# Kernel tuning notes

Hardware: AMD Instinct MI355X
Metric: run time of the kernel (lower is better)

The kernel has to match this reference:

```python
import jax, jax.numpy as jnp
import numpy as np

N = 50000        # nodes
E = 400000       # edges
SC = 64          # scalar (l=0) channels
VC = 32          # vector (l=1) channels
DIM = SC + 3 * VC  # 160
NB = 64          # radial basis functions
CUTOFF = 5.0
EPS = 1e-5


def _edge_rot_mat(edge_vec, edge_rand):
    # init_edge_rot_mat: build per-edge frame aligning edge dir with canonical axis
    dist = jnp.sqrt(jnp.sum(edge_vec ** 2, axis=1, keepdims=True))
    nx = edge_vec / dist
    ev2 = edge_rand - 0.5
    ev2 = ev2 / jnp.sqrt(jnp.sum(ev2 ** 2, axis=1, keepdims=True))
    ev2b = jnp.stack([-ev2[:, 1], ev2[:, 0], ev2[:, 2]], axis=1)
    ev2c = jnp.stack([ev2[:, 0], -ev2[:, 2], ev2[:, 1]], axis=1)
    dot = lambda a: jnp.abs(jnp.sum(a * nx, axis=1, keepdims=True))
    ev2 = jnp.where(dot(ev2) > dot(ev2b), ev2b, ev2)
    ev2 = jnp.where(dot(ev2) > dot(ev2c), ev2c, ev2)
    nz = jnp.cross(nx, ev2)
    nz = nz / jnp.sqrt(jnp.sum(nz ** 2, axis=1, keepdims=True))
    ny = jnp.cross(nx, nz)
    ny = ny / jnp.sqrt(jnp.sum(ny ** 2, axis=1, keepdims=True))
    # edge_rot_mat_inv columns = [nz, nx, -ny]; R = inv^T -> rows = [nz, nx, -ny]
    return jnp.stack([nz, nx, -ny], axis=1)  # [E,3,3]


def setup_inputs() -> dict:
    key = jax.random.key(0)
    ks = jax.random.split(key, 10)
    x = jax.random.normal(ks[0], (N, DIM), dtype=jnp.float32)
    pos = jax.random.normal(ks[1], (N, 3), dtype=jnp.float32)
    src = jax.random.randint(ks[2], (E,), 0, N)
    off = jax.random.randint(ks[3], (E,), 1, N)
    dst = (src + off) % N  # no self loops -> nonzero edge vectors
    edge_index = jnp.stack([src, dst], axis=0).astype(jnp.int64)
    edge_rand = jax.random.uniform(ks[4], (E, 3), dtype=jnp.float32)
    W0 = jax.random.normal(ks[5], (SC, SC), dtype=jnp.float32)
    W1 = jax.random.normal(ks[6], (VC, VC), dtype=jnp.float32)
    rbf_centers = jnp.linspace(0.0, CUTOFF, NB).astype(jnp.float32)
    rbf_widths = 0.5 * jnp.ones((NB,), dtype=jnp.float32)
    edge_proj_w = 0.1 * jax.random.normal(ks[7], (NB, 1), dtype=jnp.float32)
    edge_proj_b = jnp.zeros((1,), dtype=jnp.float32)
    ln_gamma = jnp.ones((SC,), dtype=jnp.float32) + 0.1 * jax.random.normal(ks[8], (SC,), dtype=jnp.float32)
    ln_beta = 0.1 * jax.random.normal(ks[9], (SC,), dtype=jnp.float32)
    return {"x": x, "pos": pos, "edge_index": edge_index, "edge_rand": edge_rand,
            "W0": W0, "W1": W1, "rbf_centers": rbf_centers, "rbf_widths": rbf_widths,
            "edge_proj_w": edge_proj_w, "edge_proj_b": edge_proj_b,
            "ln_gamma": ln_gamma, "ln_beta": ln_beta}


def reference(x, pos, edge_index, edge_rand, W0, W1, rbf_centers, rbf_widths,
              edge_proj_w, edge_proj_b, ln_gamma, ln_beta):
    src, dst = edge_index[0], edge_index[1]
    edge_vec = pos[src] - pos[dst]                       # [E,3]
    dist = jnp.sqrt(jnp.sum(edge_vec ** 2, axis=1))      # [E]
    # rotation matrices are detached in the original
    R = jax.lax.stop_gradient(_edge_rot_mat(edge_vec, edge_rand))  # [E,3,3]

    # radial basis (gaussian) with cosine cutoff envelope
    d = dist[:, None]                                    # [E,1]
    rbf = jnp.exp(-0.5 * ((d - rbf_centers) / rbf_widths) ** 2)  # [E,NB]
    cut = jnp.where(d <= CUTOFF, 0.5 * (jnp.cos(jnp.pi * d / CUTOFF) + 1.0), 0.0)
    rbf = rbf * cut                                      # [E,NB]

    # gather source features, split irreps 64x0e + 32x1e
    h = x[src]                                           # [E,DIM]
    h0 = h[:, :SC]                                       # [E,SC]
    h1 = h[:, SC:].reshape(-1, VC, 3)                    # [E,VC,3]

    # rotate l=1 block into the edge-aligned frame (Wigner-D for l=1 is R)
    h1r = jnp.einsum('eij,ecj->eci', R, h1)

    # SO2 convolution: per-l channel mixing (o3.Linear, 1/sqrt(fan_in) path norm)
    m0 = (h0 @ W0) / np.sqrt(SC)                         # [E,SC]
    m1 = jnp.einsum('ecj,cd->edj', h1r, W1) / np.sqrt(VC)  # [E,VC,3]

    # edge modulation: global mean of sigmoid(edge_proj(rbf)) (scalar, as in source)
    edge_w = jnp.mean(jax.nn.sigmoid(rbf @ edge_proj_w + edge_proj_b))
    m0 = m0 * edge_w
    m1 = m1 * edge_w

    # rotate l=1 back with R^T
    m1b = jnp.einsum('eji,ecj->eci', R, m1)
    msg = jnp.concatenate([m0, m1b.reshape(-1, 3 * VC)], axis=1)  # [E,DIM]

    # scatter-sum aggregation over destination nodes
    agg = jax.ops.segment_sum(msg, dst, num_segments=x.shape[0])  # [N,DIM]

    # EquivariantLayerNormV2: LayerNorm on l=0 slice only
    s = agg[:, :SC]
    mu = jnp.mean(s, axis=-1, keepdims=True)
    var = jnp.mean((s - mu) ** 2, axis=-1, keepdims=True)
    s_ln = (s - mu) / jnp.sqrt(var + EPS) * ln_gamma + ln_beta

    # S2Activation: SiLU on l=0 slice, identity on l=1
    s_act = jax.nn.silu(s_ln)
    return jnp.concatenate([s_act, agg[:, SC:]], axis=1)  # [N,DIM]
```

## Files before the change

kernel.cpp:

```cpp
#include <hip/hip_runtime.h>

#define N_NODES 50000
#define N_EDGES 400000
#define DIM 160
#define NB 64
#define CUTOFF 5.0f
#define LN_EPS 1e-5f
#define PI_F 3.14159265358979323846f

#define SLOT_STRIDE 64
#define DEG_STRIDE 8

#define WS_DEG   16
#define WS_PKT   (WS_DEG + N_NODES * DEG_STRIDE)
#define WS_POS4  (WS_PKT + 4 * NB)
#define WS_ESRC  (WS_POS4 + 4 * N_NODES)

__global__ __launch_bounds__(256) void prep(
    const float* __restrict__ pos, const float* __restrict__ centers,
    const float* __restrict__ widths, const float* __restrict__ proj_w,
    int* __restrict__ degp, float4* __restrict__ pkt,
    float4* __restrict__ pos4, float* __restrict__ ew_accum)
{
    const int i = blockIdx.x * blockDim.x + threadIdx.x;
    if (i < 16) ((int*)ew_accum)[i] = 0;
    if (i < NB)
        pkt[i] = make_float4(centers[i], 1.0f / widths[i], proj_w[i], 0.0f);
    if (i < N_NODES) {
        const int4 z4 = make_int4(0, 0, 0, 0);
        ((int4*)(degp))[2 * i]     = z4;
        ((int4*)(degp))[2 * i + 1] = z4;
        pos4[i] = make_float4(pos[3 * i], pos[3 * i + 1], pos[3 * i + 2], 0.0f);
    }
}

#define EPT 4

__global__ __launch_bounds__(256) void hist_ew_fill(
    const int* __restrict__ ei, const float4* __restrict__ pos4,
    const float4* __restrict__ pkt, const float* __restrict__ proj_b,
    int* __restrict__ degp, int* __restrict__ esrc, float* __restrict__ ew_accum)
{
    const float bias = proj_b[0];
    const int base = blockIdx.x * (256 * EPT) + threadIdx.x;

    int  s[EPT], d[EPT], slot[EPT];
    bool v[EPT];
    #pragma unroll
    for (int k = 0; k < EPT; ++k) {
        const int e = base + 256 * k;
        v[k] = (e < N_EDGES);
        s[k] = v[k] ? ei[e] : 0;
        d[k] = v[k] ? ei[N_EDGES + e] : 0;
    }

    #pragma unroll
    for (int k = 0; k < EPT; ++k)
        slot[k] = v[k] ? atomicAdd(&degp[(long)d[k] * DEG_STRIDE], 1) : 0;

    float4 ps[EPT], pd[EPT];
    #pragma unroll
    for (int k = 0; k < EPT; ++k) { ps[k] = pos4[s[k]]; pd[k] = pos4[d[k]]; }

    #pragma unroll
    for (int k = 0; k < EPT; ++k)
        if (v[k] && slot[k] < SLOT_STRIDE)
            esrc[((long)d[k] << 6) + slot[k]] = s[k];

    float dist[EPT];
    #pragma unroll
    for (int k = 0; k < EPT; ++k) {
        const float dx = ps[k].x - pd[k].x;
        const float dy = ps[k].y - pd[k].y;
        const float dz = ps[k].z - pd[k].z;
        dist[k] = sqrtf(dx * dx + dy * dy + dz * dz);
    }

    float z[EPT] = {0.f, 0.f, 0.f, 0.f};
    #pragma unroll 4
    for (int b = 0; b < NB; ++b) {
        const float4 t4 = pkt[b];
        #pragma unroll
        for (int k = 0; k < EPT; ++k) {
            const float t = (dist[k] - t4.x) * t4.y;
            z[k] = fmaf(__expf(-0.5f * t * t), t4.z, z[k]);
        }
    }

    float sig = 0.0f;
    #pragma unroll
    for (int k = 0; k < EPT; ++k) {
        if (v[k]) {
            const float cut = (dist[k] <= CUTOFF)
                            ? 0.5f * (__cosf(PI_F * dist[k] * (1.0f / CUTOFF)) + 1.0f)
                            : 0.0f;
            sig += 1.0f / (1.0f + __expf(-(z[k] * cut + bias)));
        }
    }

    #pragma unroll
    for (int off = 32; off > 0; off >>= 1) sig += __shfl_xor(sig, off);
    __shared__ float red[4];
    if ((threadIdx.x & 63) == 0) red[threadIdx.x >> 6] = sig;
    __syncthreads();
    if (threadIdx.x == 0)
        atomicAdd(ew_accum, red[0] + red[1] + red[2] + red[3]);
}

#define TNODES 16

__global__ __launch_bounds__(256) void gather_node(
    const float* __restrict__ x, const int* __restrict__ degp,
    const int* __restrict__ esrc, float* __restrict__ out,
    const float* __restrict__ W0, const float* __restrict__ W1,
    const float* __restrict__ ln_gamma, const float* __restrict__ ln_beta,
    const float* __restrict__ ew_accum)
{
    __shared__ float sW0[64 * 64];
    __shared__ float sW1[32 * 32];
    __shared__ float sRow[4][2][160];

    const int t    = threadIdx.x;
    const int lane = t & 63;
    const int w    = t >> 6;
    const int node0 = blockIdx.x * TNODES;

    {
        const float4* w04 = (const float4*)W0;
        float4* s04 = (float4*)sW0;
        #pragma unroll
        for (int i = 0; i < 4; ++i) s04[t + 256 * i] = w04[t + 256 * i];
        ((float4*)sW1)[t] = ((const float4*)W1)[t];
    }
    __syncthreads();

    const float ew   = ew_accum[0] * (1.0f / 400000.0f);
    const float s_m0 = ew * 0.125f;
    const float s_m1 = ew * 0.17677669529663687f;

    const int half = lane >> 5;
    const int l    = lane & 31;

    #pragma unroll 1
    for (int p = 0; p < 4; p += 2) {
        const int nA  = node0 + 4 * w + p;
        const int nB  = nA + 1;
        const long nAc = (nA < N_NODES) ? nA : 0;
        const long nBc = (nB < N_NODES) ? nB : 0;

        const int svA  = esrc[(nAc << 6) + lane];
        const int svB  = esrc[(nBc << 6) + lane];
        const int cntA = (nA < N_NODES) ? min(degp[nAc * DEG_STRIDE], SLOT_STRIDE) : 0;
        const int cntB = (nB < N_NODES) ? min(degp[nBc * DEG_STRIDE], SLOT_STRIDE) : 0;

        float4 aA = make_float4(0.f, 0.f, 0.f, 0.f);
        float4 aB = make_float4(0.f, 0.f, 0.f, 0.f);

        #define GBODY(sv, cnt, acc)                                            \
        {                                                                      \
            int j = 0;                                                         \
            for (; j + 8 <= cnt; j += 8) {                                     \
                const int s0 = __shfl(sv, j);                                  \
                const int s1 = __shfl(sv, j + 1);                              \
                const int s2 = __shfl(sv, j + 2);                              \
                const int s3 = __shfl(sv, j + 3);                              \
                const int s4 = __shfl(sv, j + 4);                              \
                const int s5 = __shfl(sv, j + 5);                              \
                const int s6 = __shfl(sv, j + 6);                              \
                const int s7 = __shfl(sv, j + 7);                              \
                if (lane < 40) {                                               \
                    const float4 v0 = ((const float4*)(x + (long)s0 * DIM))[lane]; \
                    const float4 v1 = ((const float4*)(x + (long)s1 * DIM))[lane]; \
                    const float4 v2 = ((const float4*)(x + (long)s2 * DIM))[lane]; \
                    const float4 v3 = ((const float4*)(x + (long)s3 * DIM))[lane]; \
                    const float4 v4 = ((const float4*)(x + (long)s4 * DIM))[lane]; \
                    const float4 v5 = ((const float4*)(x + (long)s5 * DIM))[lane]; \
                    const float4 v6 = ((const float4*)(x + (long)s6 * DIM))[lane]; \
                    const float4 v7 = ((const float4*)(x + (long)s7 * DIM))[lane]; \
                    acc.x += ((v0.x + v1.x) + (v2.x + v3.x)) + ((v4.x + v5.x) + (v6.x + v7.x)); \
                    acc.y += ((v0.y + v1.y) + (v2.y + v3.y)) + ((v4.y + v5.y) + (v6.y + v7.y)); \
                    acc.z += ((v0.z + v1.z) + (v2.z + v3.z)) + ((v4.z + v5.z) + (v6.z + v7.z)); \
                    acc.w += ((v0.w + v1.w) + (v2.w + v3.w)) + ((v4.w + v5.w) + (v6.w + v7.w)); \
                }                                                              \
            }                                                                  \
            for (; j + 4 <= cnt; j += 4) {                                     \
                const int s0 = __shfl(sv, j);                                  \
                const int s1 = __shfl(sv, j + 1);                              \
                const int s2 = __shfl(sv, j + 2);                              \
                const int s3 = __shfl(sv, j + 3);                              \
                if (lane < 40) {                                               \
                    const float4 v0 = ((const float4*)(x + (long)s0 * DIM))[lane]; \
                    const float4 v1 = ((const float4*)(x + (long)s1 * DIM))[lane]; \
                    const float4 v2 = ((const float4*)(x + (long)s2 * DIM))[lane]; \
                    const float4 v3 = ((const float4*)(x + (long)s3 * DIM))[lane]; \
                    acc.x += (v0.x + v1.x) + (v2.x + v3.x);                    \
                    acc.y += (v0.y + v1.y) + (v2.y + v3.y);                    \
                    acc.z += (v0.z + v1.z) + (v2.z + v3.z);                    \
                    acc.w += (v0.w + v1.w) + (v2.w + v3.w);                    \
                }                                                              \
            }                                                                  \
            for (; j < cnt; ++j) {                                             \
                const int s0 = __shfl(sv, j);                                  \
                if (lane < 40) {                                               \
                    const float4 v0 = ((const float4*)(x + (long)s0 * DIM))[lane]; \
                    acc.x += v0.x; acc.y += v0.y; acc.z += v0.z; acc.w += v0.w; \
                }                                                              \
            }                                                                  \
        }
        GBODY(svA, cntA, aA)
        GBODY(svB, cntB, aB)
        #undef GBODY

        if (lane < 40) {
            *(float4*)(&sRow[w][0][4 * lane]) = aA;
            *(float4*)(&sRow[w][1][4 * lane]) = aB;
        }

        const int  node  = node0 + 4 * w + p + half;
        const bool valid = node < N_NODES;
        float* grow = out + (long)(valid ? node : 0) * DIM;
        const float* row = &sRow[w][half][0];

        {
            float a0 = 0.f, a1 = 0.f;
            #pragma unroll 4
            for (int k0 = 0; k0 < 64; k0 += 4) {
                const float4 a = *(const float4*)(row + k0);
                const float2 q0 = *(const float2*)(sW0 + (k0 + 0) * 64 + 2 * l);
                const float2 q1 = *(const float2*)(sW0 + (k0 + 1) * 64 + 2 * l);
                const float2 q2 = *(const float2*)(sW0 + (k0 + 2) * 64 + 2 * l);
                const float2 q3 = *(const float2*)(sW0 + (k0 + 3) * 64 + 2 * l);
                a0 = fmaf(a.x, q0.x, fmaf(a.y, q1.x, fmaf(a.z, q2.x, fmaf(a.w, q3.x, a0))));
                a1 = fmaf(a.x, q0.y, fmaf(a.y, q1.y, fmaf(a.z, q2.y, fmaf(a.w, q3.y, a1))));
            }
            a0 *= s_m0;
            a1 *= s_m0;

            float sum = a0 + a1;
            float ssq = fmaf(a0, a0, a1 * a1);
            #pragma unroll
            for (int m = 1; m <= 16; m <<= 1) {
                sum += __shfl_xor(sum, m);
                ssq += __shfl_xor(ssq, m);
            }

            if (valid) {
                const float mu   = sum * (1.0f / 64.0f);
                const float var  = ssq * (1.0f / 64.0f) - mu * mu;
                const float rstd = rsqrtf(var + LN_EPS);
                const float2 g = *(const float2*)(ln_gamma + 2 * l);
                const float2 b = *(const float2*)(ln_beta  + 2 * l);
                const float t0 = (a0 - mu) * rstd * g.x + b.x;
                const float t1 = (a1 - mu) * rstd * g.y + b.y;
                float2 o;
                o.x = t0 / (1.0f + __expf(-t0));
                o.y = t1 / (1.0f + __expf(-t1));
                *(float2*)(grow + 2 * l) = o;
            }
        }

        {
            const float* vrow = row + 64;
            float o0 = 0.f, o1 = 0.f, o2 = 0.f;
            #pragma unroll 2
            for (int g = 0; g < 8; ++g) {
                const float4 v0 = *(const float4*)(vrow + 12 * g);
                const float4 v1 = *(const float4*)(vrow + 12 * g + 4);
                const float4 v2 = *(const float4*)(vrow + 12 * g + 8);
                const float a[12] = { v0.x, v0.y, v0.z, v0.w,
                                      v1.x, v1.y, v1.z, v1.w,
                                      v2.x, v2.y, v2.z, v2.w };
                #pragma unroll
                for (int r = 0; r < 4; ++r) {
                    const float wc = sW1[(4 * g + r) * 32 + l];
                    o0 = fmaf(wc, a[3 * r],     o0);
                    o1 = fmaf(wc, a[3 * r + 1], o1);
                    o2 = fmaf(wc, a[3 * r + 2], o2);
                }
            }
            if (valid) {
                float* vo = grow + 64 + 3 * l;
                vo[0] = o0 * s_m1;
                vo[1] = o1 * s_m1;
                vo[2] = o2 * s_m1;
            }
        }
    }
}

extern "C" void kernel_launch(void* const* d_in, const int* in_sizes, int n_in,
                              void* d_out, int out_size, void* d_ws, size_t ws_size,
                              hipStream_t stream) {
    const float* x       = (const float*)d_in[0];
    const float* pos     = (const float*)d_in[1];
    const int*   ei      = (const int*)d_in[2];
    const float* W0      = (const float*)d_in[4];
    const float* W1      = (const float*)d_in[5];
    const float* centers = (const float*)d_in[6];
    const float* widths  = (const float*)d_in[7];
    const float* proj_w  = (const float*)d_in[8];
    const float* proj_b  = (const float*)d_in[9];
    const float* gamma   = (const float*)d_in[10];
    const float* beta    = (const float*)d_in[11];

    float* out  = (float*)d_out;
    int*   wsi  = (int*)d_ws;
    float* ew   = (float*)d_ws;
    int*   degp = wsi + WS_DEG;
    float4* pkt  = (float4*)(wsi + WS_PKT);
    float4* pos4 = (float4*)(wsi + WS_POS4);
    int*   esrc = wsi + WS_ESRC;

    const int pb = (N_NODES + 255) / 256;
    prep<<<pb, 256, 0, stream>>>(pos, centers, widths, proj_w, degp, pkt, pos4, ew);

    const int eb = (N_EDGES + 256 * EPT - 1) / (256 * EPT);
    hist_ew_fill<<<eb, 256, 0, stream>>>(ei, pos4, pkt, proj_b, degp, esrc, ew);

    const int tiles = (N_NODES + TNODES - 1) / TNODES;
    gather_node<<<tiles, 256, 0, stream>>>(x, degp, esrc, out,
                                           W0, W1, gamma, beta, ew);
}
```

Measured before the change: 180.7 us.

## Interleave neighbor gathers of node pairs with masked fixed-width batches

The per-node gather is restructured so that all four nodes' edge lists and degrees are loaded up front, and pairs of nodes are gathered together in masked batches of 8. This keeps 16 row loads in flight per iteration instead of handling each node's loop serially with remainder tails. The aim is more memory-level parallelism and fewer serial latency chains. The cost is wasted loads of row 0 for padded slots when the two degrees differ, plus higher register pressure and a larger shared-memory staging buffer. The matmul and normalization passes now read from the pre-gathered rows.

```diff
diff --git a/kernel.cpp b/kernel.cpp
--- a/kernel.cpp
+++ b/kernel.cpp
@@ -118,12 +118,13 @@
 {
     __shared__ float sW0[64 * 64];
     __shared__ float sW1[32 * 32];
-    __shared__ float sRow[4][2][160];
+    __shared__ float sRow[4][4][160];
 
     const int t    = threadIdx.x;
     const int lane = t & 63;
     const int w    = t >> 6;
     const int node0 = blockIdx.x * TNODES;
+    const int nbase = node0 + 4 * w;
 
     {
         const float4* w04 = (const float4*)W0;
@@ -138,88 +139,77 @@
     const float s_m0 = ew * 0.125f;
     const float s_m1 = ew * 0.17677669529663687f;
 
+    int sv[4], cnt[4];
+    #pragma unroll
+    for (int k = 0; k < 4; ++k) {
+        const int n = nbase + k;
+        const long nc = (n < N_NODES) ? n : 0;
+        sv[k]  = esrc[(nc << 6) + lane];
+        cnt[k] = (n < N_NODES) ? min(degp[nc * DEG_STRIDE], SLOT_STRIDE) : 0;
+    }
+
+    float4 acc[4];
+    #pragma unroll
+    for (int k = 0; k < 4; ++k) acc[k] = make_float4(0.f, 0.f, 0.f, 0.f);
+
+    #define GPAIR(kA, kB)                                                      \
+    {                                                                          \
+        const int mx = max(cnt[kA], cnt[kB]);                                  \
+        for (int j = 0; j < mx; j += 8) {                                      \
+            int   sa[8], sb[8];                                                \
+            float ma[8], mb[8];                                                \
+            _Pragma("unroll")                                                  \
+            for (int i = 0; i < 8; ++i) {                                      \
+                const bool va = (j + i) < cnt[kA];                             \
+                const bool vb = (j + i) < cnt[kB];                             \
+                const int ra = __shfl(sv[kA], j + i);                          \
+                const int rb = __shfl(sv[kB], j + i);                          \
+                sa[i] = va ? ra : 0;                                           \
+                sb[i] = vb ? rb : 0;                                           \
+                ma[i] = va ? 1.0f : 0.0f;                                      \
+                mb[i] = vb ? 1.0f : 0.0f;                                      \
+            }                                                                  \
+            if (lane < 40) {                                                   \
+                float4 va4[8], vb4[8];                                         \
+                _Pragma("unroll")                                              \
+                for (int i = 0; i < 8; ++i)                                    \
+                    va4[i] = ((const float4*)(x + (long)sa[i] * DIM))[lane];   \
+                _Pragma("unroll")                                              \
+                for (int i = 0; i < 8; ++i)                                    \
+                    vb4[i] = ((const float4*)(x + (long)sb[i] * DIM))[lane];   \
+                _Pragma("unroll")                                              \
+                for (int i = 0; i < 8; ++i) {                                  \
+                    acc[kA].x = fmaf(ma[i], va4[i].x, acc[kA].x);              \
+                    acc[kA].y = fmaf(ma[i], va4[i].y, acc[kA].y);              \
+                    acc[kA].z = fmaf(ma[i], va4[i].z, acc[kA].z);              \
+                    acc[kA].w = fmaf(ma[i], va4[i].w, acc[kA].w);              \
+                    acc[kB].x = fmaf(mb[i], vb4[i].x, acc[kB].x);              \
+                    acc[kB].y = fmaf(mb[i], vb4[i].y, acc[kB].y);              \
+                    acc[kB].z = fmaf(mb[i], vb4[i].z, acc[kB].z);              \
+                    acc[kB].w = fmaf(mb[i], vb4[i].w, acc[kB].w);              \
+                }                                                              \
+            }                                                                  \
+        }                                                                      \
+    }
+    GPAIR(0, 1)
+    GPAIR(2, 3)
+    #undef GPAIR
+
+    if (lane < 40) {
+        #pragma unroll
+        for (int k = 0; k < 4; ++k)
+            *(float4*)(&sRow[w][k][4 * lane]) = acc[k];
+    }
+
     const int half = lane >> 5;
     const int l    = lane & 31;
 
     #pragma unroll 1
-    for (int p = 0; p < 4; p += 2) {
-        const int nA  = node0 + 4 * w + p;
-        const int nB  = nA + 1;
-        const long nAc = (nA < N_NODES) ? nA : 0;
-        const long nBc = (nB < N_NODES) ? nB : 0;
-
-        const int svA  = esrc[(nAc << 6) + lane];
-        const int svB  = esrc[(nBc << 6) + lane];
-        const int cntA = (nA < N_NODES) ? min(degp[nAc * DEG_STRIDE], SLOT_STRIDE) : 0;
-        const int cntB = (nB < N_NODES) ? min(degp[nBc * DEG_STRIDE], SLOT_STRIDE) : 0;
-
-        float4 aA = make_float4(0.f, 0.f, 0.f, 0.f);
-        float4 aB = make_float4(0.f, 0.f, 0.f, 0.f);
-
-        #define GBODY(sv, cnt, acc)                                            \
-        {                                                                      \
-            int j = 0;                                                         \
-            for (; j + 8 <= cnt; j += 8) {                                     \
-                const int s0 = __shfl(sv, j);                                  \
-                const int s1 = __shfl(sv, j + 1);                              \
-                const int s2 = __shfl(sv, j + 2);                              \
-                const int s3 = __shfl(sv, j + 3);                              \
-                const int s4 = __shfl(sv, j + 4);                              \
-                const int s5 = __shfl(sv, j + 5);                              \
-                const int s6 = __shfl(sv, j + 6);                              \
-                const int s7 = __shfl(sv, j + 7);                              \
-                if (lane < 40) {                                               \
-                    const float4 v0 = ((const float4*)(x + (long)s0 * DIM))[lane]; \
-                    const float4 v1 = ((const float4*)(x + (long)s1 * DIM))[lane]; \
-                    const float4 v2 = ((const float4*)(x + (long)s2 * DIM))[lane]; \
-                    const float4 v3 = ((const float4*)(x + (long)s3 * DIM))[lane]; \
-                    const float4 v4 = ((const float4*)(x + (long)s4 * DIM))[lane]; \
-                    const float4 v5 = ((const float4*)(x + (long)s5 * DIM))[lane]; \
-                    const float4 v6 = ((const float4*)(x + (long)s6 * DIM))[lane]; \
-                    const float4 v7 = ((const float4*)(x + (long)s7 * DIM))[lane]; \
-                    acc.x += ((v0.x + v1.x) + (v2.x + v3.x)) + ((v4.x + v5.x) + (v6.x + v7.x)); \
-                    acc.y += ((v0.y + v1.y) + (v2.y + v3.y)) + ((v4.y + v5.y) + (v6.y + v7.y)); \
-                    acc.z += ((v0.z + v1.z) + (v2.z + v3.z)) + ((v4.z + v5.z) + (v6.z + v7.z)); \
-                    acc.w += ((v0.w + v1.w) + (v2.w + v3.w)) + ((v4.w + v5.w) + (v6.w + v7.w)); \
-                }                                                              \
-            }                                                                  \
-            for (; j + 4 <= cnt; j += 4) {                                     \
-                const int s0 = __shfl(sv, j);                                  \
-                const int s1 = __shfl(sv, j + 1);                              \
-                const int s2 = __shfl(sv, j + 2);                              \
-                const int s3 = __shfl(sv, j + 3);                              \
-                if (lane < 40) {                                               \
-                    const float4 v0 = ((const float4*)(x + (long)s0 * DIM))[lane]; \
-                    const float4 v1 = ((const float4*)(x + (long)s1 * DIM))[lane]; \
-                    const float4 v2 = ((const float4*)(x + (long)s2 * DIM))[lane]; \
-                    const float4 v3 = ((const float4*)(x + (long)s3 * DIM))[lane]; \
-                    acc.x += (v0.x + v1.x) + (v2.x + v3.x);                    \
-                    acc.y += (v0.y + v1.y) + (v2.y + v3.y);                    \
-                    acc.z += (v0.z + v1.z) + (v2.z + v3.z);                    \
-                    acc.w += (v0.w + v1.w) + (v2.w + v3.w);                    \
-                }                                                              \
-            }                                                                  \
-            for (; j < cnt; ++j) {                                             \
-                const int s0 = __shfl(sv, j);                                  \
-                if (lane < 40) {                                               \
-                    const float4 v0 = ((const float4*)(x + (long)s0 * DIM))[lane]; \
-                    acc.x += v0.x; acc.y += v0.y; acc.z += v0.z; acc.w += v0.w; \
-                }                                                              \
-            }                                                                  \
-        }
-        GBODY(svA, cntA, aA)
-        GBODY(svB, cntB, aB)
-        #undef GBODY
-
-        if (lane < 40) {
-            *(float4*)(&sRow[w][0][4 * lane]) = aA;
-            *(float4*)(&sRow[w][1][4 * lane]) = aB;
-        }
-
-        const int  node  = node0 + 4 * w + p + half;
+    for (int pass = 0; pass < 2; ++pass) {
+        const int  node  = nbase + 2 * pass + half;
         const bool valid = node < N_NODES;
         float* grow = out + (long)(valid ? node : 0) * DIM;
-        const float* row = &sRow[w][half][0];
+        const float* row = &sRow[w][2 * pass + half][0];
 
         {
             float a0 = 0.f, a1 = 0.f;
```

Result: no change. 181.8 us (+0.6%).
